# Kernel tuning notes

Hardware: AMD Instinct MI355X
Metric: run time of the kernel (lower is better)

## Reference

```python
import jax, jax.numpy as jnp
import numpy as np


def setup_inputs() -> dict:
    key = jax.random.key(0)
    kx, kw = jax.random.split(key)
    x = jax.random.normal(kx, (16, 256, 128, 128), dtype=jnp.float32)
    weight = jax.random.normal(kw, (128, 256, 3, 3), dtype=jnp.float32)
    return {"x": x, "weight": weight}


def reference(x, weight):
    # alpha = mean(|W|) per output channel, shape [Cout] (matches E.squeeze())
    alpha = jnp.mean(jnp.abs(weight), axis=(1, 2, 3))
    binary_weight = jnp.sign(weight)
    binary_input = jnp.sign(x)
    out = jax.lax.conv_general_dilated(
        binary_input, binary_weight,
        window_strides=(1, 1),
        padding=((1, 1), (1, 1)),
        dimension_numbers=("NCHW", "OIHW", "NCHW"),
    )  # [N, Cout, H, W] with W == Cout by construction
    # Faithful to torch: `output * alpha` broadcasts alpha[Cout] along the
    # LAST (width) axis, which equals Cout for the chosen shapes.
    return out * alpha
```

## Files before the change

kernel.cpp:

```cpp
#include <hip/hip_runtime.h>
#include <stdint.h>

#define CIN   256
#define COUT  128
#define HH    128
#define WW    128
#define NIMG  16

typedef unsigned long long u64;
typedef unsigned int u32;
typedef unsigned short u16;
typedef u32 u32x4 __attribute__((ext_vector_type(4)));
typedef int i32x4 __attribute__((ext_vector_type(4)));
typedef int i32x16 __attribute__((ext_vector_type(16)));
typedef signed char i8;

__global__ __launch_bounds__(256) void pack_x_kernel(const float* __restrict__ x,
                                                     u64* __restrict__ px) {
    int t = blockIdx.x * 256 + threadIdx.x;
    int w = t & (WW - 1);
    int h = (t >> 7) & (HH - 1);
    int n = t >> 14;
    const float* xp = x + (size_t)n * CIN * HH * WW + (size_t)h * WW + w;
    u64 words[4];
#pragma unroll
    for (int wd = 0; wd < 4; ++wd) {
        u64 acc = 0;
#pragma unroll 16
        for (int cc = 0; cc < 64; ++cc) {
            float v = xp[(size_t)(wd * 64 + cc) * (HH * WW)];
            acc |= (u64)(v > 0.0f) << cc;
        }
        words[wd] = acc;
    }
    ulonglong2* o = reinterpret_cast<ulonglong2*>(px + (size_t)t * 4);
    o[0] = make_ulonglong2(words[0], words[1]);
    o[1] = make_ulonglong2(words[2], words[3]);
}

__global__ __launch_bounds__(256) void pack_w_kernel(const float* __restrict__ wt,
                                                     i8* __restrict__ wg,
                                                     short* __restrict__ wsum,
                                                     float* __restrict__ alpha) {
    int co = blockIdx.x;
    int c  = threadIdx.x;
    int lane = c & 63;
    int word = c >> 6;
    __shared__ u64 wsh[9][4];
    __shared__ int pct[9];
    __shared__ float red[4];
    const float* wp = wt + ((size_t)co * CIN + c) * 9;
    float asum = 0.0f;
#pragma unroll
    for (int k = 0; k < 9; ++k) {
        float v = wp[k];
        asum += fabsf(v);
        u64 m = __ballot(v > 0.0f);
        if (lane == 0) wsh[k][word] = m;
        int k16g = k * 16 + (c >> 4);
        wg[((size_t)k16g * COUT + co) * 16 + (c & 15)] = (v > 0.0f) ? (i8)1 : (i8)-1;
    }
    for (int off = 32; off > 0; off >>= 1) asum += __shfl_down(asum, off);
    if (lane == 0) red[word] = asum;
    __syncthreads();
    if (c < 9)
        pct[c] = __popcll(wsh[c][0]) + __popcll(wsh[c][1]) +
                 __popcll(wsh[c][2]) + __popcll(wsh[c][3]);
    if (c == 0) alpha[co] = (red[0] + red[1] + red[2] + red[3]) * (1.0f / 2304.0f);
    __syncthreads();
    if (c < 9) {
        int pat = c, ht = pat / 3, wtp = pat % 3;
        int s = 0;
#pragma unroll
        for (int k = 0; k < 9; ++k) {
            int dh = k / 3 - 1, dw = k % 3 - 1;
            bool inv = (dh == -1 && ht == 0) || (dh == 1 && ht == 2) ||
                       (dw == -1 && wtp == 0) || (dw == 1 && wtp == 2);
            if (!inv) s += 2 * pct[k] - 256;
        }
        wsum[pat * COUT + co] = (short)s;
    }
}

__device__ __forceinline__ i32x4 spread16(u32 v) {
    u32 o0 = (((v      ) & 15u) * 0x00204081u) & 0x01010101u;
    u32 o1 = (((v >>  4) & 15u) * 0x00204081u) & 0x01010101u;
    u32 o2 = (((v >>  8) & 15u) * 0x00204081u) & 0x01010101u;
    u32 o3 = (((v >> 12) & 15u) * 0x00204081u) & 0x01010101u;
    i32x4 r = {(int)o0, (int)o1, (int)o2, (int)o3};
    return r;
}

__global__ __launch_bounds__(256, 4) void conv_kernel(const u64* __restrict__ px,
                                                      const i8* __restrict__ wg,
                                                      const short* __restrict__ wsum,
                                                      const float* __restrict__ alpha,
                                                      float* __restrict__ out) {
    __shared__ u16 xlt[3][16][130];
    __shared__ short wsl[9 * COUT];
    __shared__ float alds[WW];

    int tid = threadIdx.x;
    int bid = blockIdx.x;
    int h = bid & (HH - 1);
    int n = bid >> 7;

    if (tid < WW) alds[tid] = alpha[tid];
    {
        const u32* s = reinterpret_cast<const u32*>(wsum);
        u32* d = reinterpret_cast<u32*>(wsl);
        for (int i = tid; i < 9 * COUT / 2; i += 256) d[i] = s[i];
    }

    for (int t = tid; t < 390; t += 256) {
        int r = (t >= 260) ? 2 : ((t >= 130) ? 1 : 0);
        int p = t - r * 130;
        int gh = h - 1 + r;
        u32 bw[8] = {0, 0, 0, 0, 0, 0, 0, 0};
        if ((p >= 1) && (p <= 128) && (gh >= 0) && (gh < HH)) {
            const u32x4* s = reinterpret_cast<const u32x4*>(
                px + (size_t)((n * HH + gh) * WW + (p - 1)) * 4);
            u32x4 a = s[0], b = s[1];
            bw[0] = a.x; bw[1] = a.y; bw[2] = a.z; bw[3] = a.w;
            bw[4] = b.x; bw[5] = b.y; bw[6] = b.z; bw[7] = b.w;
        }
#pragma unroll
        for (int k16 = 0; k16 < 16; ++k16)
            xlt[r][k16][p] = (u16)(bw[k16 >> 1] >> ((k16 & 1) * 16));
    }
    __syncthreads();

    int lane = tid & 63;
    int wave = tid >> 6;
    int l31 = lane & 31;
    int hi  = lane >> 5;
    int co0  = (wave & 1) * 64;
    int pos0 = (wave >> 1) * 64;

    i32x16 accA0 = {}, accA1 = {}, accB0 = {}, accB1 = {};

#pragma unroll 1
    for (int ch = 0; ch < 18; ++ch) {
        int tap = ch >> 1;
        int k16b = (ch & 1) * 8;
        int r   = tap / 3;
        int dwi = tap - r * 3;
        int colA = pos0 + l31 + dwi;
        int colB = colA + 32;
        int k16gb = tap * 16 + k16b;
#pragma unroll
        for (int ks = 0; ks < 4; ++ks) {
            int k16 = k16b + ks * 2 + hi;
            i32x4 xfA = spread16((u32)xlt[r][k16][colA]);
            i32x4 xfB = spread16((u32)xlt[r][k16][colB]);
            int k16g = k16gb + ks * 2 + hi;
            const i32x4* wp = reinterpret_cast<const i32x4*>(
                wg + ((size_t)k16g * COUT) * 16);
            i32x4 wf0 = wp[co0 + l31];
            i32x4 wf1 = wp[co0 + 32 + l31];
            accA0 = __builtin_amdgcn_mfma_i32_32x32x32_i8(wf0, xfA, accA0, 0, 0, 0);
            accA1 = __builtin_amdgcn_mfma_i32_32x32x32_i8(wf1, xfA, accA1, 0, 0, 0);
            accB0 = __builtin_amdgcn_mfma_i32_32x32x32_i8(wf0, xfB, accB0, 0, 0, 0);
            accB1 = __builtin_amdgcn_mfma_i32_32x32x32_i8(wf1, xfB, accB1, 0, 0, 0);
        }
    }

    int hpat = (h == 0) ? 0 : ((h == HH - 1) ? 2 : 1);
#pragma unroll
    for (int half = 0; half < 2; ++half) {
        int wcol = pos0 + half * 32 + l31;
        float aw = alds[wcol];
        int wpat = (wcol == 0) ? 0 : ((wcol == WW - 1) ? 2 : 1);
        const short* wsp = &wsl[(hpat * 3 + wpat) * COUT];
        i32x16 a0 = half ? accB0 : accA0;
        i32x16 a1 = half ? accB1 : accA1;
#pragma unroll
        for (int reg = 0; reg < 16; ++reg) {
            int rr = (reg & 3) + 8 * (reg >> 2) + 4 * hi;
            int coa = co0 + rr;
            int cob = co0 + 32 + rr;
            out[((size_t)(n * COUT + coa) * HH + h) * WW + wcol] =
                (float)(2 * a0[reg] - (int)wsp[coa]) * aw;
            out[((size_t)(n * COUT + cob) * HH + h) * WW + wcol] =
                (float)(2 * a1[reg] - (int)wsp[cob]) * aw;
        }
    }
}

extern "C" void kernel_launch(void* const* d_in, const int* in_sizes, int n_in,
                              void* d_out, int out_size, void* d_ws, size_t ws_size,
                              hipStream_t stream) {
    const float* x  = (const float*)d_in[0];
    const float* wt = (const float*)d_in[1];
    float* out = (float*)d_out;

    char* ws = (char*)d_ws;
    const size_t PX_BYTES = (size_t)NIMG * HH * WW * 4 * sizeof(u64);
    const size_t WG_BYTES = (size_t)144 * COUT * 16;
    const size_t WS_BYTES = (size_t)9 * COUT * sizeof(short);
    const size_t AL_BYTES = 512;
    if (ws_size < PX_BYTES + WG_BYTES + WS_BYTES + AL_BYTES) return;
    u64*   px    = (u64*)ws;
    i8*    wg    = (i8*)(ws + PX_BYTES);
    short* wsum  = (short*)(ws + PX_BYTES + WG_BYTES);
    float* alpha = (float*)(ws + PX_BYTES + WG_BYTES + WS_BYTES);

    pack_x_kernel<<<NIMG * HH * WW / 256, 256, 0, stream>>>(x, px);
    pack_w_kernel<<<COUT, 256, 0, stream>>>(wt, wg, wsum, alpha);
    conv_kernel<<<NIMG * HH, 256, 0, stream>>>(px, wg, wsum, alpha, out);
}
```

Before: 150.2 us.

## Retile conv waves to cover all output channels over 32 positions each

Changes the per-wave tile from 64 channels by 64 positions to all 128 channels by 32 positions. Each wave now unpacks one activation fragment per k-step instead of two, but loads four weight fragments from global instead of two. The bit-spread multiply also switches to 24-bit multiplies. This cuts the VALU spread work and LDS reads per MFMA, at the cost of more global/L2 weight traffic per wave.

```diff
diff --git a/kernel.cpp b/kernel.cpp
--- a/kernel.cpp
+++ b/kernel.cpp
@@ -83,10 +83,10 @@
 }
 
 __device__ __forceinline__ i32x4 spread16(u32 v) {
-    u32 o0 = (((v      ) & 15u) * 0x00204081u) & 0x01010101u;
-    u32 o1 = (((v >>  4) & 15u) * 0x00204081u) & 0x01010101u;
-    u32 o2 = (((v >>  8) & 15u) * 0x00204081u) & 0x01010101u;
-    u32 o3 = (((v >> 12) & 15u) * 0x00204081u) & 0x01010101u;
+    u32 o0 = __umul24((v      ) & 15u, 0x00204081u) & 0x01010101u;
+    u32 o1 = __umul24((v >>  4) & 15u, 0x00204081u) & 0x01010101u;
+    u32 o2 = __umul24((v >>  8) & 15u, 0x00204081u) & 0x01010101u;
+    u32 o3 = __umul24((v >> 12) & 15u, 0x00204081u) & 0x01010101u;
     i32x4 r = {(int)o0, (int)o1, (int)o2, (int)o3};
     return r;
 }
@@ -134,10 +134,9 @@
     int wave = tid >> 6;
     int l31 = lane & 31;
     int hi  = lane >> 5;
-    int co0  = (wave & 1) * 64;
-    int pos0 = (wave >> 1) * 64;
-
-    i32x16 accA0 = {}, accA1 = {}, accB0 = {}, accB1 = {};
+    int pos0 = wave * 32;
+
+    i32x16 acc0 = {}, acc1 = {}, acc2 = {}, acc3 = {};
 
 #pragma unroll 1
     for (int ch = 0; ch < 18; ++ch) {
@@ -145,45 +144,38 @@
         int k16b = (ch & 1) * 8;
         int r   = tap / 3;
         int dwi = tap - r * 3;
-        int colA = pos0 + l31 + dwi;
-        int colB = colA + 32;
-        int k16gb = tap * 16 + k16b;
+        int col = pos0 + l31 + dwi;
 #pragma unroll
         for (int ks = 0; ks < 4; ++ks) {
             int k16 = k16b + ks * 2 + hi;
-            i32x4 xfA = spread16((u32)xlt[r][k16][colA]);
-            i32x4 xfB = spread16((u32)xlt[r][k16][colB]);
-            int k16g = k16gb + ks * 2 + hi;
+            i32x4 xf = spread16((u32)xlt[r][k16][col]);
+            int k16g = tap * 16 + k16;
             const i32x4* wp = reinterpret_cast<const i32x4*>(
                 wg + ((size_t)k16g * COUT) * 16);
-            i32x4 wf0 = wp[co0 + l31];
-            i32x4 wf1 = wp[co0 + 32 + l31];
-            accA0 = __builtin_amdgcn_mfma_i32_32x32x32_i8(wf0, xfA, accA0, 0, 0, 0);
-            accA1 = __builtin_amdgcn_mfma_i32_32x32x32_i8(wf1, xfA, accA1, 0, 0, 0);
-            accB0 = __builtin_amdgcn_mfma_i32_32x32x32_i8(wf0, xfB, accB0, 0, 0, 0);
-            accB1 = __builtin_amdgcn_mfma_i32_32x32x32_i8(wf1, xfB, accB1, 0, 0, 0);
+            i32x4 wf0 = wp[l31];
+            i32x4 wf1 = wp[32 + l31];
+            i32x4 wf2 = wp[64 + l31];
+            i32x4 wf3 = wp[96 + l31];
+            acc0 = __builtin_amdgcn_mfma_i32_32x32x32_i8(wf0, xf, acc0, 0, 0, 0);
+            acc1 = __builtin_amdgcn_mfma_i32_32x32x32_i8(wf1, xf, acc1, 0, 0, 0);
+            acc2 = __builtin_amdgcn_mfma_i32_32x32x32_i8(wf2, xf, acc2, 0, 0, 0);
+            acc3 = __builtin_amdgcn_mfma_i32_32x32x32_i8(wf3, xf, acc3, 0, 0, 0);
         }
     }
 
     int hpat = (h == 0) ? 0 : ((h == HH - 1) ? 2 : 1);
-#pragma unroll
-    for (int half = 0; half < 2; ++half) {
-        int wcol = pos0 + half * 32 + l31;
-        float aw = alds[wcol];
-        int wpat = (wcol == 0) ? 0 : ((wcol == WW - 1) ? 2 : 1);
-        const short* wsp = &wsl[(hpat * 3 + wpat) * COUT];
-        i32x16 a0 = half ? accB0 : accA0;
-        i32x16 a1 = half ? accB1 : accA1;
-#pragma unroll
-        for (int reg = 0; reg < 16; ++reg) {
-            int rr = (reg & 3) + 8 * (reg >> 2) + 4 * hi;
-            int coa = co0 + rr;
-            int cob = co0 + 32 + rr;
-            out[((size_t)(n * COUT + coa) * HH + h) * WW + wcol] =
-                (float)(2 * a0[reg] - (int)wsp[coa]) * aw;
-            out[((size_t)(n * COUT + cob) * HH + h) * WW + wcol] =
-                (float)(2 * a1[reg] - (int)wsp[cob]) * aw;
-        }
+    int wcol = pos0 + l31;
+    float aw = alds[wcol];
+    int wpat = (wcol == 0) ? 0 : ((wcol == WW - 1) ? 2 : 1);
+    const short* wsp = &wsl[(hpat * 3 + wpat) * COUT];
+    float* ob = out + ((size_t)n * COUT * HH + h) * WW + wcol;
+#pragma unroll
+    for (int reg = 0; reg < 16; ++reg) {
+        int rr = (reg & 3) + 8 * (reg >> 2) + 4 * hi;
+        ob[(size_t)(rr)       * (HH * WW)] = (float)(2 * acc0[reg] - (int)wsp[rr])       * aw;
+        ob[(size_t)(rr + 32)  * (HH * WW)] = (float)(2 * acc1[reg] - (int)wsp[rr + 32])  * aw;
+        ob[(size_t)(rr + 64)  * (HH * WW)] = (float)(2 * acc2[reg] - (int)wsp[rr + 64])  * aw;
+        ob[(size_t)(rr + 96)  * (HH * WW)] = (float)(2 * acc3[reg] - (int)wsp[rr + 96])  * aw;
     }
 }
 
```

After: 170.0 us. 1.13x slower.

## Software-pipeline weight fragment loads in conv kernel with double-buffered registers

Applied to the files above, without the earlier changes.

Restructures the MFMA main loop so that weight fragments for the next chunk are loaded from global memory into a second register buffer while the current chunk computes, hiding global-load latency behind MFMAs. Occupancy hint lowered from 4 to 3 waves per SIMD to give room for the extra 16 vector registers of weight fragments. Also uses 24-bit multiplies in the bit-spread helper. Risks lower occupancy and higher register pressure.

```diff
diff --git a/kernel.cpp b/kernel.cpp
--- a/kernel.cpp
+++ b/kernel.cpp
@@ -83,15 +83,35 @@
 }
 
 __device__ __forceinline__ i32x4 spread16(u32 v) {
-    u32 o0 = (((v      ) & 15u) * 0x00204081u) & 0x01010101u;
-    u32 o1 = (((v >>  4) & 15u) * 0x00204081u) & 0x01010101u;
-    u32 o2 = (((v >>  8) & 15u) * 0x00204081u) & 0x01010101u;
-    u32 o3 = (((v >> 12) & 15u) * 0x00204081u) & 0x01010101u;
+    u32 o0 = __umul24((v      ) & 15u, 0x00204081u) & 0x01010101u;
+    u32 o1 = __umul24((v >>  4) & 15u, 0x00204081u) & 0x01010101u;
+    u32 o2 = __umul24((v >>  8) & 15u, 0x00204081u) & 0x01010101u;
+    u32 o3 = __umul24((v >> 12) & 15u, 0x00204081u) & 0x01010101u;
     i32x4 r = {(int)o0, (int)o1, (int)o2, (int)o3};
     return r;
 }
 
-__global__ __launch_bounds__(256, 4) void conv_kernel(const u64* __restrict__ px,
+#define COMPUTE_CHUNK(CH, WREG)                                               \
+    {                                                                         \
+        int tap  = (CH) >> 1;                                                 \
+        int k16b = ((CH) & 1) * 8;                                            \
+        int r    = tap / 3;                                                   \
+        int dwi  = tap - r * 3;                                               \
+        int colA = pos0 + l31 + dwi;                                          \
+        int colB = colA + 32;                                                 \
+        _Pragma("unroll")                                                     \
+        for (int ks = 0; ks < 4; ++ks) {                                      \
+            int k16 = k16b + ks * 2 + hi;                                     \
+            i32x4 xfA = spread16((u32)xlt[r][k16][colA]);                     \
+            i32x4 xfB = spread16((u32)xlt[r][k16][colB]);                     \
+            accA0 = __builtin_amdgcn_mfma_i32_32x32x32_i8(WREG[2*ks],   xfA, accA0, 0, 0, 0); \
+            accA1 = __builtin_amdgcn_mfma_i32_32x32x32_i8(WREG[2*ks+1], xfA, accA1, 0, 0, 0); \
+            accB0 = __builtin_amdgcn_mfma_i32_32x32x32_i8(WREG[2*ks],   xfB, accB0, 0, 0, 0); \
+            accB1 = __builtin_amdgcn_mfma_i32_32x32x32_i8(WREG[2*ks+1], xfB, accB1, 0, 0, 0); \
+        }                                                                     \
+    }
+
+__global__ __launch_bounds__(256, 3) void conv_kernel(const u64* __restrict__ px,
                                                       const i8* __restrict__ wg,
                                                       const short* __restrict__ wsum,
                                                       const float* __restrict__ alpha,
@@ -139,31 +159,38 @@
 
     i32x16 accA0 = {}, accA1 = {}, accB0 = {}, accB1 = {};
 
+    const i8* wgb = wg + ((size_t)co0 + l31) * 16;
+#define WFRAG(CH, KS, SEL)                                                    \
+    (*reinterpret_cast<const i32x4*>(wgb +                                    \
+        (size_t)(((CH) >> 1) * 16 + ((CH) & 1) * 8 + (KS) * 2 + hi) * 2048 +  \
+        (SEL) * 512))
+
+    i32x4 wA[8], wB[8];
+#pragma unroll
+    for (int ks = 0; ks < 4; ++ks) {
+        wA[2 * ks]     = WFRAG(0, ks, 0);
+        wA[2 * ks + 1] = WFRAG(0, ks, 1);
+    }
+
 #pragma unroll 1
-    for (int ch = 0; ch < 18; ++ch) {
-        int tap = ch >> 1;
-        int k16b = (ch & 1) * 8;
-        int r   = tap / 3;
-        int dwi = tap - r * 3;
-        int colA = pos0 + l31 + dwi;
-        int colB = colA + 32;
-        int k16gb = tap * 16 + k16b;
+    for (int ch2 = 0; ch2 < 9; ++ch2) {
+        int chA = 2 * ch2, chB = 2 * ch2 + 1;
 #pragma unroll
         for (int ks = 0; ks < 4; ++ks) {
-            int k16 = k16b + ks * 2 + hi;
-            i32x4 xfA = spread16((u32)xlt[r][k16][colA]);
-            i32x4 xfB = spread16((u32)xlt[r][k16][colB]);
-            int k16g = k16gb + ks * 2 + hi;
-            const i32x4* wp = reinterpret_cast<const i32x4*>(
-                wg + ((size_t)k16g * COUT) * 16);
-            i32x4 wf0 = wp[co0 + l31];
-            i32x4 wf1 = wp[co0 + 32 + l31];
-            accA0 = __builtin_amdgcn_mfma_i32_32x32x32_i8(wf0, xfA, accA0, 0, 0, 0);
-            accA1 = __builtin_amdgcn_mfma_i32_32x32x32_i8(wf1, xfA, accA1, 0, 0, 0);
-            accB0 = __builtin_amdgcn_mfma_i32_32x32x32_i8(wf0, xfB, accB0, 0, 0, 0);
-            accB1 = __builtin_amdgcn_mfma_i32_32x32x32_i8(wf1, xfB, accB1, 0, 0, 0);
-        }
-    }
+            wB[2 * ks]     = WFRAG(chB, ks, 0);
+            wB[2 * ks + 1] = WFRAG(chB, ks, 1);
+        }
+        COMPUTE_CHUNK(chA, wA);
+        if (ch2 < 8) {
+#pragma unroll
+            for (int ks = 0; ks < 4; ++ks) {
+                wA[2 * ks]     = WFRAG(chA + 2, ks, 0);
+                wA[2 * ks + 1] = WFRAG(chA + 2, ks, 1);
+            }
+        }
+        COMPUTE_CHUNK(chB, wB);
+    }
+#undef WFRAG
 
     int hpat = (h == 0) ? 0 : ((h == HH - 1) ? 2 : 1);
 #pragma unroll
```

Result: faster. 146.9 us (-2.2%).

## Bit-pack binary weights and stage them in LDS, expanding to ±1 bytes in-register

Applied to the files above, without the earlier changes.

Weights are now stored as 16-bit sign masks, 36 KB instead of 295 KB of int8, and copied into shared memory per block. Inside the MFMA loop they are expanded to ±1 int8 with multiply/mask and v_perm, so the per-iteration global weight loads go away. Activation spreading switches to 24-bit multiplies. In exchange the loop does more ALU work and uses more LDS per block, so the occupancy hint drops from 4 to 3 blocks.

```diff
diff --git a/kernel.cpp b/kernel.cpp
--- a/kernel.cpp
+++ b/kernel.cpp
@@ -39,7 +39,7 @@
 }
 
 __global__ __launch_bounds__(256) void pack_w_kernel(const float* __restrict__ wt,
-                                                     i8* __restrict__ wg,
+                                                     u16* __restrict__ wq,
                                                      short* __restrict__ wsum,
                                                      float* __restrict__ alpha) {
     int co = blockIdx.x;
@@ -57,8 +57,13 @@
         asum += fabsf(v);
         u64 m = __ballot(v > 0.0f);
         if (lane == 0) wsh[k][word] = m;
-        int k16g = k * 16 + (c >> 4);
-        wg[((size_t)k16g * COUT + co) * 16 + (c & 15)] = (v > 0.0f) ? (i8)1 : (i8)-1;
+        if ((c & 15) == 0) {
+            int rbit = c & 63;
+            int j = rbit >> 4;
+            u32 bits = (u32)((m >> rbit) & 0xFFFFull);
+            int k16g = k * 16 + word * 4 + j;
+            wq[(size_t)(k16g >> 1) * 256 + co * 2 + (k16g & 1)] = (u16)bits;
+        }
     }
     for (int off = 32; off > 0; off >>= 1) asum += __shfl_down(asum, off);
     if (lane == 0) red[word] = asum;
@@ -83,20 +88,34 @@
 }
 
 __device__ __forceinline__ i32x4 spread16(u32 v) {
-    u32 o0 = (((v      ) & 15u) * 0x00204081u) & 0x01010101u;
-    u32 o1 = (((v >>  4) & 15u) * 0x00204081u) & 0x01010101u;
-    u32 o2 = (((v >>  8) & 15u) * 0x00204081u) & 0x01010101u;
-    u32 o3 = (((v >> 12) & 15u) * 0x00204081u) & 0x01010101u;
+    u32 o0 = __umul24((v      ) & 15u, 0x00204081u) & 0x01010101u;
+    u32 o1 = __umul24((v >>  4) & 15u, 0x00204081u) & 0x01010101u;
+    u32 o2 = __umul24((v >>  8) & 15u, 0x00204081u) & 0x01010101u;
+    u32 o3 = __umul24((v >> 12) & 15u, 0x00204081u) & 0x01010101u;
     i32x4 r = {(int)o0, (int)o1, (int)o2, (int)o3};
     return r;
 }
 
-__global__ __launch_bounds__(256, 4) void conv_kernel(const u64* __restrict__ px,
-                                                      const i8* __restrict__ wg,
+__device__ __forceinline__ i32x4 expandpm16(u32 v) {
+    u32 s0 = __umul24((v      ) & 15u, 0x00810204u) & 0x04040404u;
+    u32 s1 = __umul24((v >>  4) & 15u, 0x00810204u) & 0x04040404u;
+    u32 s2 = __umul24((v >>  8) & 15u, 0x00810204u) & 0x04040404u;
+    u32 s3 = __umul24((v >> 12) & 15u, 0x00810204u) & 0x04040404u;
+    u32 o0 = __builtin_amdgcn_perm(0x01010101u, 0xFFFFFFFFu, s0);
+    u32 o1 = __builtin_amdgcn_perm(0x01010101u, 0xFFFFFFFFu, s1);
+    u32 o2 = __builtin_amdgcn_perm(0x01010101u, 0xFFFFFFFFu, s2);
+    u32 o3 = __builtin_amdgcn_perm(0x01010101u, 0xFFFFFFFFu, s3);
+    i32x4 r = {(int)o0, (int)o1, (int)o2, (int)o3};
+    return r;
+}
+
+__global__ __launch_bounds__(256, 3) void conv_kernel(const u64* __restrict__ px,
+                                                      const u32* __restrict__ wq32,
                                                       const short* __restrict__ wsum,
                                                       const float* __restrict__ alpha,
                                                       float* __restrict__ out) {
     __shared__ u16 xlt[3][16][130];
+    __shared__ u32 wql[72 * 128];
     __shared__ short wsl[9 * COUT];
     __shared__ float alds[WW];
 
@@ -111,6 +130,7 @@
         u32* d = reinterpret_cast<u32*>(wsl);
         for (int i = tid; i < 9 * COUT / 2; i += 256) d[i] = s[i];
     }
+    for (int i = tid; i < 72 * 128; i += 256) wql[i] = wq32[i];
 
     for (int t = tid; t < 390; t += 256) {
         int r = (t >= 260) ? 2 : ((t >= 130) ? 1 : 0);
@@ -147,17 +167,15 @@
         int dwi = tap - r * 3;
         int colA = pos0 + l31 + dwi;
         int colB = colA + 32;
-        int k16gb = tap * 16 + k16b;
+        int kpb = tap * 8 + (ch & 1) * 4;
 #pragma unroll
         for (int ks = 0; ks < 4; ++ks) {
             int k16 = k16b + ks * 2 + hi;
             i32x4 xfA = spread16((u32)xlt[r][k16][colA]);
             i32x4 xfB = spread16((u32)xlt[r][k16][colB]);
-            int k16g = k16gb + ks * 2 + hi;
-            const i32x4* wp = reinterpret_cast<const i32x4*>(
-                wg + ((size_t)k16g * COUT) * 16);
-            i32x4 wf0 = wp[co0 + l31];
-            i32x4 wf1 = wp[co0 + 32 + l31];
+            const u16* wrow = reinterpret_cast<const u16*>(&wql[(kpb + ks) * 128]);
+            i32x4 wf0 = expandpm16((u32)wrow[(co0 + l31) * 2 + hi]);
+            i32x4 wf1 = expandpm16((u32)wrow[(co0 + 32 + l31) * 2 + hi]);
             accA0 = __builtin_amdgcn_mfma_i32_32x32x32_i8(wf0, xfA, accA0, 0, 0, 0);
             accA1 = __builtin_amdgcn_mfma_i32_32x32x32_i8(wf1, xfA, accA1, 0, 0, 0);
             accB0 = __builtin_amdgcn_mfma_i32_32x32x32_i8(wf0, xfB, accB0, 0, 0, 0);
@@ -196,16 +214,16 @@
 
     char* ws = (char*)d_ws;
     const size_t PX_BYTES = (size_t)NIMG * HH * WW * 4 * sizeof(u64);
-    const size_t WG_BYTES = (size_t)144 * COUT * 16;
+    const size_t WQ_BYTES = (size_t)72 * 128 * sizeof(u32);
     const size_t WS_BYTES = (size_t)9 * COUT * sizeof(short);
     const size_t AL_BYTES = 512;
-    if (ws_size < PX_BYTES + WG_BYTES + WS_BYTES + AL_BYTES) return;
+    if (ws_size < PX_BYTES + WQ_BYTES + WS_BYTES + AL_BYTES) return;
     u64*   px    = (u64*)ws;
-    i8*    wg    = (i8*)(ws + PX_BYTES);
-    short* wsum  = (short*)(ws + PX_BYTES + WG_BYTES);
-    float* alpha = (float*)(ws + PX_BYTES + WG_BYTES + WS_BYTES);
+    u16*   wq    = (u16*)(ws + PX_BYTES);
+    short* wsum  = (short*)(ws + PX_BYTES + WQ_BYTES);
+    float* alpha = (float*)(ws + PX_BYTES + WQ_BYTES + WS_BYTES);
 
     pack_x_kernel<<<NIMG * HH * WW / 256, 256, 0, stream>>>(x, px);
-    pack_w_kernel<<<COUT, 256, 0, stream>>>(wt, wg, wsum, alpha);
-    conv_kernel<<<NIMG * HH, 256, 0, stream>>>(px, wg, wsum, alpha, out);
-}
+    pack_w_kernel<<<COUT, 256, 0, stream>>>(wt, wq, wsum, alpha);
+    conv_kernel<<<NIMG * HH, 256, 0, stream>>>(px, (const u32*)wq, wsum, alpha, out);
+}
```

Result: slower. 159.8 us (+6.4%).
